# Kernel tuning notes

Measured on AMD Instinct MI355X. Metric: run time of the kernel, lower is better.

Reference implementation:

```python
import jax, jax.numpy as jnp
import numpy as np

B, L, D_MODEL, N_HEADS = 4, 2048, 1024, 16
HEAD_DIM = D_MODEL // N_HEADS


def setup_inputs() -> dict:
    key = jax.random.key(0)
    ks = jax.random.split(key, 11)
    s = 1.0 / np.sqrt(D_MODEL)
    return {
        "queries": jax.random.normal(ks[0], (B, L, D_MODEL), jnp.float32),
        "keys": jax.random.normal(ks[1], (B, L, D_MODEL), jnp.float32),
        "values": jax.random.normal(ks[2], (B, L, D_MODEL), jnp.float32),
        "Wq": jax.random.normal(ks[3], (D_MODEL, D_MODEL), jnp.float32) * s,
        "bq": jnp.zeros((D_MODEL,), jnp.float32),
        "Wk": jax.random.normal(ks[4], (D_MODEL, D_MODEL), jnp.float32) * s,
        "bk": jnp.zeros((D_MODEL,), jnp.float32),
        "Wv": jax.random.normal(ks[5], (D_MODEL, D_MODEL), jnp.float32) * s,
        "bv": jnp.zeros((D_MODEL,), jnp.float32),
        "Wo": jax.random.normal(ks[6], (D_MODEL, D_MODEL), jnp.float32) * s,
        "bo": jnp.zeros((D_MODEL,), jnp.float32),
    }


def reference(queries, keys, values, Wq, bq, Wk, bk, Wv, bv, Wo, bo):
    Bsz, Lq, _ = queries.shape
    S = keys.shape[1]
    H, E = N_HEADS, HEAD_DIM
    # QKV projections (weights stored [in, out])
    q = (queries @ Wq + bq).reshape(Bsz, Lq, H, E)
    k = (keys @ Wk + bk).reshape(Bsz, S, H, E)
    v = (values @ Wv + bv).reshape(Bsz, S, H, E)
    scale = 1.0 / np.sqrt(E)
    # scores: [B, H, L, S]
    scores = jnp.einsum("blhe,bshe->bhls", q, k)
    A = jax.nn.softmax(scale * scores, axis=-1)
    # context: [B, L, H, E] -> [B, L, D]
    ctx = jnp.einsum("bhls,bshd->blhd", A, v).reshape(Bsz, Lq, H * E)
    out = ctx @ Wo + bo
    return out
```

## Files before the change

### kernel.cpp

```cpp
#include <hip/hip_runtime.h>

#define BATCH 4
#define SEQ   2048
#define DMODEL 1024
#define NHEADS 16
#define HDIM  64
#define MROWS (BATCH * SEQ)

typedef float f32x4 __attribute__((ext_vector_type(4)));
typedef short s16x8 __attribute__((ext_vector_type(8)));
typedef short s16x4 __attribute__((ext_vector_type(4)));
typedef unsigned short u16;

#define MFMA32K(a, b, c) __builtin_amdgcn_mfma_f32_16x16x32_bf16((a), (b), (c), 0, 0, 0)
#define MFMA16K(a, b, c) __builtin_amdgcn_mfma_f32_16x16x16bf16_1k((a), (b), (c), 0, 0, 0)

__device__ __forceinline__ u16 f2bf(float x) {
    unsigned int u = __builtin_bit_cast(unsigned int, x);
    unsigned int r = u + 0x7fffu + ((u >> 16) & 1u);
    return (u16)(r >> 16);
}

#if __has_builtin(__builtin_amdgcn_cvt_pk_bf16_f32)
__device__ __forceinline__ unsigned int pack2bf(float a, float b) {
    auto r = __builtin_amdgcn_cvt_pk_bf16_f32(a, b);
    return __builtin_bit_cast(unsigned int, r);
}
#else
__device__ __forceinline__ unsigned int pack2bf(float a, float b) {
    return (unsigned int)f2bf(a) | ((unsigned int)f2bf(b) << 16);
}
#endif

__device__ __forceinline__ void dma16(const u16* g, const u16* l) {
    __builtin_amdgcn_global_load_lds(
        (const __attribute__((address_space(1))) unsigned int*)g,
        (__attribute__((address_space(3))) unsigned int*)l, 16, 0, 0);
}

__global__ __launch_bounds__(256) void convk3(
    const float* __restrict__ s0, const float* __restrict__ s1,
    const float* __restrict__ s2, u16* __restrict__ d0, u16* __restrict__ d1,
    u16* __restrict__ d2) {
    const int z = blockIdx.y;
    const float* src = (z == 0) ? s0 : (z == 1) ? s1 : s2;
    u16* dst = (z == 0) ? d0 : (z == 1) ? d1 : d2;
    const int i = blockIdx.x * 256 + threadIdx.x;
    float4 a = ((const float4*)src)[i * 2];
    float4 b = ((const float4*)src)[i * 2 + 1];
    uint4 o;
    o.x = pack2bf(a.x, a.y); o.y = pack2bf(a.z, a.w);
    o.z = pack2bf(b.x, b.y); o.w = pack2bf(b.z, b.w);
    *(uint4*)(dst + (size_t)i * 8) = o;
}

__global__ __launch_bounds__(256) void wconv(const float* __restrict__ W0,
                                             const float* __restrict__ W1,
                                             const float* __restrict__ W2,
                                             const float* __restrict__ W3,
                                             u16* __restrict__ Wt) {
    __shared__ u16 tile[64][80];
    const int t = threadIdx.x;
    const int mtx = blockIdx.z;
    const float* W = (mtx == 0) ? W0 : (mtx == 1) ? W1 : (mtx == 2) ? W2 : W3;
    u16* out = Wt + (size_t)mtx * DMODEL * DMODEL;
    const int n0 = blockIdx.x * 64, k0 = blockIdx.y * 64;
#pragma unroll
    for (int j = 0; j < 4; ++j) {
        int k = j * 16 + (t >> 4);
        int c = (t & 15) * 4;
        float4 v = *(const float4*)(W + (size_t)(k0 + k) * DMODEL + n0 + c);
        tile[c + 0][k] = f2bf(v.x);
        tile[c + 1][k] = f2bf(v.y);
        tile[c + 2][k] = f2bf(v.z);
        tile[c + 3][k] = f2bf(v.w);
    }
    __syncthreads();
#pragma unroll
    for (int i2 = 0; i2 < 2; ++i2) {
        int n = i2 * 32 + (t >> 3), ck = (t & 7) * 8;
        uint4 v = *(const uint4*)(&tile[n][ck]);
        *(uint4*)(out + (size_t)(n0 + n) * DMODEL + k0 + ck) = v;
    }
}

__global__ __launch_bounds__(256) void vtrans(const u16* __restrict__ vbuf,
                                              u16* __restrict__ vtg) {
    __shared__ u16 tile[64][72];
    const int t = threadIdx.x;
    const int s0 = blockIdx.x * 64, h = blockIdx.y, b = blockIdx.z;
#pragma unroll
    for (int i = 0; i < 2; ++i) {
        int idx = i * 256 + t;
        int srow = idx >> 3, un = idx & 7;
        union { uint4 v; u16 s[8]; } u;
        u.v = *(const uint4*)(vbuf + (size_t)(b * SEQ + s0 + srow) * DMODEL + h * HDIM + un * 8);
#pragma unroll
        for (int ii = 0; ii < 8; ++ii)
            tile[un * 8 + ii][srow] = u.s[ii];
    }
    __syncthreads();
#pragma unroll
    for (int i = 0; i < 2; ++i) {
        int idx = i * 256 + t;
        int e = idx >> 3, un = idx & 7;
        uint4 v = *(const uint4*)(&tile[e][un * 8]);
        *(uint4*)(vtg + ((size_t)((b * NHEADS + h) * HDIM + e)) * SEQ + s0 + un * 8) = v;
    }
}

__global__ __launch_bounds__(256) void gemm_qkv(
    const u16* __restrict__ Aq, const u16* __restrict__ Ak,
    const u16* __restrict__ Av, const u16* __restrict__ Wt,
    const float* __restrict__ biq, const float* __restrict__ bik,
    const float* __restrict__ biv, u16* __restrict__ oq, u16* __restrict__ ok,
    u16* __restrict__ ov, float sq) {
    __shared__ u16 As[128 * 32];
    __shared__ u16 Bs[128 * 32];
    const int t = threadIdx.x;
    const int w = t >> 6, lane = t & 63, quad = lane >> 4, l16 = lane & 15;
    const int z = blockIdx.z;
    const u16* A = (z == 0) ? Aq : (z == 1) ? Ak : Av;
    const u16* B = Wt + (size_t)z * DMODEL * DMODEL;
    const float* bias = (z == 0) ? biq : (z == 1) ? bik : biv;
    u16* C = (z == 0) ? oq : (z == 1) ? ok : ov;
    const float scale = (z == 0) ? sq : 1.0f;
    const int m0 = blockIdx.x * 128, n0 = blockIdx.y * 128;
    const int wm = (w >> 1) * 64, wn = (w & 1) * 64;
    const int lr = lane >> 2, lc = (lane & 3) * 8;

    f32x4 acc[4][4] = {};

    for (int k0 = 0; k0 < DMODEL; k0 += 32) {
#pragma unroll
        for (int j = 0; j < 2; ++j) {
            int row = w * 32 + j * 16;
            dma16(A + (size_t)(m0 + row + lr) * DMODEL + k0 + lc, &As[row * 32]);
            dma16(B + (size_t)(n0 + row + lr) * DMODEL + k0 + lc, &Bs[row * 32]);
        }
        __syncthreads();
        s16x8 af[4], bf[4];
#pragma unroll
        for (int mt = 0; mt < 4; ++mt)
            af[mt] = *(const s16x8*)(&As[(wm + mt * 16 + l16) * 32 + quad * 8]);
#pragma unroll
        for (int nt = 0; nt < 4; ++nt)
            bf[nt] = *(const s16x8*)(&Bs[(wn + nt * 16 + l16) * 32 + quad * 8]);
#pragma unroll
        for (int mt = 0; mt < 4; ++mt)
#pragma unroll
            for (int nt = 0; nt < 4; ++nt)
                acc[mt][nt] = MFMA32K(af[mt], bf[nt], acc[mt][nt]);
        __syncthreads();
    }

#pragma unroll
    for (int mt = 0; mt < 4; ++mt)
#pragma unroll
        for (int nt = 0; nt < 4; ++nt) {
            int col = n0 + wn + nt * 16 + l16;
            float bv_ = bias[col];
#pragma unroll
            for (int r = 0; r < 4; ++r) {
                int row = m0 + wm + mt * 16 + quad * 4 + r;
                C[(size_t)row * DMODEL + col] = f2bf((acc[mt][nt][r] + bv_) * scale);
            }
        }
}

__global__ __launch_bounds__(256) void gemm_o(const u16* __restrict__ A,
                                              const u16* __restrict__ Bt,
                                              const float* __restrict__ bias,
                                              float* __restrict__ Cp) {
    __shared__ u16 As[128 * 32];
    __shared__ u16 Bs[128 * 32];
    const int t = threadIdx.x;
    const int w = t >> 6, lane = t & 63, quad = lane >> 4, l16 = lane & 15;
    const int m0 = blockIdx.x * 128, n0 = blockIdx.y * 128;
    const int wm = (w >> 1) * 64, wn = (w & 1) * 64;
    const int lr = lane >> 2, lc = (lane & 3) * 8;

    f32x4 acc[4][4] = {};

    for (int k0 = 0; k0 < DMODEL; k0 += 32) {
#pragma unroll
        for (int j = 0; j < 2; ++j) {
            int row = w * 32 + j * 16;
            dma16(A + (size_t)(m0 + row + lr) * DMODEL + k0 + lc, &As[row * 32]);
            dma16(Bt + (size_t)(n0 + row + lr) * DMODEL + k0 + lc, &Bs[row * 32]);
        }
        __syncthreads();
        s16x8 af[4], bf[4];
#pragma unroll
        for (int mt = 0; mt < 4; ++mt)
            af[mt] = *(const s16x8*)(&As[(wm + mt * 16 + l16) * 32 + quad * 8]);
#pragma unroll
        for (int nt = 0; nt < 4; ++nt)
            bf[nt] = *(const s16x8*)(&Bs[(wn + nt * 16 + l16) * 32 + quad * 8]);
#pragma unroll
        for (int mt = 0; mt < 4; ++mt)
#pragma unroll
            for (int nt = 0; nt < 4; ++nt)
                acc[mt][nt] = MFMA32K(af[mt], bf[nt], acc[mt][nt]);
        __syncthreads();
    }

#pragma unroll
    for (int mt = 0; mt < 4; ++mt)
#pragma unroll
        for (int nt = 0; nt < 4; ++nt) {
            int col = n0 + wn + nt * 16 + l16;
            float bv_ = bias[col];
#pragma unroll
            for (int r = 0; r < 4; ++r) {
                int row = m0 + wm + mt * 16 + quad * 4 + r;
                Cp[(size_t)row * DMODEL + col] = acc[mt][nt][r] + bv_;
            }
        }
}

__global__ __launch_bounds__(256, 4) void attn3(const u16* __restrict__ qb,
                                                const u16* __restrict__ kb,
                                                const u16* __restrict__ vtg,
                                                u16* __restrict__ ctxb) {
    __shared__ u16 Ks[2][64 * 64];
    __shared__ u16 Vt[2][64 * 64];
    const int t = threadIdx.x;
    const int w = t >> 6, lane = t & 63, quad = lane >> 4, l16 = lane & 15;
    const int h = blockIdx.x, b = blockIdx.z, q0 = blockIdx.y * 128;

    s16x8 bq[2][2];
#pragma unroll
    for (int qs = 0; qs < 2; ++qs) {
        size_t base = (size_t)(b * SEQ + q0 + w * 32 + qs * 16 + l16) * DMODEL + h * HDIM + quad * 8;
        bq[qs][0] = *(const s16x8*)(qb + base);
        bq[qs][1] = *(const s16x8*)(qb + base + 32);
    }

    const int krow = lane >> 3;
    const int kunit = (lane & 7) ^ krow;
    const u16* vbase = vtg + (size_t)((b * NHEADS + h) * HDIM) * SEQ;

    float lsum[2] = {0.0f, 0.0f};
    f32x4 o[2][4] = {};

#define STAGE_KV(bf_, ss_)                                                              \
    do {                                                                                \
        _Pragma("unroll")                                                               \
        for (int j = 0; j < 2; ++j) {                                                   \
            int row = w * 16 + j * 8 + krow;                                            \
            dma16(kb + (size_t)(b * SEQ + (ss_) + row) * DMODEL + h * HDIM + kunit * 8, \
                  &Ks[bf_][(w * 16 + j * 8) * 64]);                                     \
            dma16(vbase + (size_t)row * SEQ + (ss_) + kunit * 8,                        \
                  &Vt[bf_][(w * 16 + j * 8) * 64]);                                     \
        }                                                                               \
    } while (0)

    STAGE_KV(0, 0);
    __syncthreads();

    const int NT = SEQ / 64;
    for (int tt = 0; tt < NT; ++tt) {
        const int buf = tt & 1;
        if (tt + 1 < NT) STAGE_KV(buf ^ 1, (tt + 1) * 64);

        s16x8 ak[4][2];
#pragma unroll
        for (int kt = 0; kt < 4; ++kt) {
            int row = kt * 16 + l16;
#pragma unroll
            for (int hf = 0; hf < 2; ++hf) {
                int un = (hf * 4 + quad) ^ (l16 & 7);
                ak[kt][hf] = *(const s16x8*)(&Ks[buf][row * 64 + un * 8]);
            }
        }

        s16x4 pf[2][4];
#pragma unroll
        for (int qs = 0; qs < 2; ++qs) {
            f32x4 sc[4];
            __builtin_amdgcn_s_setprio(1);
#pragma unroll
            for (int kt = 0; kt < 4; ++kt) {
                f32x4 zz = {0.0f, 0.0f, 0.0f, 0.0f};
                zz = MFMA32K(ak[kt][0], bq[qs][0], zz);
                sc[kt] = MFMA32K(ak[kt][1], bq[qs][1], zz);
            }
            __builtin_amdgcn_s_setprio(0);
            float rs = 0.0f;
            float p[4][4];
#pragma unroll
            for (int kt = 0; kt < 4; ++kt)
#pragma unroll
                for (int r = 0; r < 4; ++r) {
                    p[kt][r] = __builtin_amdgcn_exp2f(sc[kt][r]);
                    rs += p[kt][r];
                }
            rs += __shfl_xor(rs, 16);
            rs += __shfl_xor(rs, 32);
            lsum[qs] += rs;
#pragma unroll
            for (int kt = 0; kt < 4; ++kt) {
                union { unsigned int u[2]; s16x4 v; } pb;
                pb.u[0] = pack2bf(p[kt][0], p[kt][1]);
                pb.u[1] = pack2bf(p[kt][2], p[kt][3]);
                pf[qs][kt] = pb.v;
            }
        }

#pragma unroll
        for (int mt = 0; mt < 4; ++mt) {
            const int dim = mt * 16 + l16;
            const u16* vrow = &Vt[buf][dim * 64 + ((quad & 1) << 2)];
            const int sw = l16 & 7;
#pragma unroll
            for (int kt = 0; kt < 4; ++kt) {
                int un = (kt * 2 + (quad >> 1)) ^ sw;
                s16x4 av = *(const s16x4*)(vrow + un * 8);
                __builtin_amdgcn_s_setprio(1);
#pragma unroll
                for (int qs = 0; qs < 2; ++qs)
                    o[qs][mt] = MFMA16K(av, pf[qs][kt], o[qs][mt]);
                __builtin_amdgcn_s_setprio(0);
            }
        }
        __syncthreads();
    }
#undef STAGE_KV

#pragma unroll
    for (int qs = 0; qs < 2; ++qs) {
        float rl = 1.0f / lsum[qs];
        size_t rowbase = (size_t)(b * SEQ + q0 + w * 32 + qs * 16 + l16) * DMODEL + h * HDIM;
#pragma unroll
        for (int mt = 0; mt < 4; ++mt)
#pragma unroll
            for (int rr = 0; rr < 2; ++rr) {
                unsigned int v = pack2bf(o[qs][mt][rr * 2] * rl, o[qs][mt][rr * 2 + 1] * rl);
                *(unsigned int*)(&ctxb[rowbase + mt * 16 + quad * 4 + rr * 2]) = v;
            }
    }
}

extern "C" void kernel_launch(void* const* d_in, const int* in_sizes, int n_in,
                              void* d_out, int out_size, void* d_ws, size_t ws_size,
                              hipStream_t stream) {
    const float* queries = (const float*)d_in[0];
    const float* keys    = (const float*)d_in[1];
    const float* values  = (const float*)d_in[2];
    const float* Wq = (const float*)d_in[3];
    const float* bq = (const float*)d_in[4];
    const float* Wk = (const float*)d_in[5];
    const float* bk = (const float*)d_in[6];
    const float* Wv = (const float*)d_in[7];
    const float* bv = (const float*)d_in[8];
    const float* Wo = (const float*)d_in[9];
    const float* bo = (const float*)d_in[10];
    float* out = (float*)d_out;

    char* ws = (char*)d_ws;
    u16* Wt   = (u16*)ws;
    u16* aq   = (u16*)(ws + ((size_t)8 << 20));
    u16* ak   = (u16*)(ws + ((size_t)24 << 20));
    u16* av   = (u16*)(ws + ((size_t)40 << 20));
    u16* qbuf = (u16*)(ws + ((size_t)56 << 20));
    u16* kbuf = (u16*)(ws + ((size_t)72 << 20));
    u16* vbuf = (u16*)(ws + ((size_t)88 << 20));
    u16* ctxb = qbuf;
    u16* vtg  = av;

    const size_t WSZ = (size_t)DMODEL * DMODEL;
    const float S2 = 0.125f * 1.44269504088896340736f;

    dim3 blk(256);

    wconv<<<dim3(16, 16, 4), blk, 0, stream>>>(Wq, Wk, Wv, Wo, Wt);
    convk3<<<dim3(4096, 3), blk, 0, stream>>>(queries, keys, values, aq, ak, av);

    gemm_qkv<<<dim3(64, 8, 3), blk, 0, stream>>>(aq, ak, av, Wt,
                                                 bq, bk, bv, qbuf, kbuf, vbuf, S2);

    vtrans<<<dim3(SEQ / 64, NHEADS, BATCH), blk, 0, stream>>>(vbuf, vtg);

    attn3<<<dim3(NHEADS, SEQ / 128, BATCH), blk, 0, stream>>>(qbuf, kbuf, vtg, ctxb);

    gemm_o<<<dim3(64, 8), blk, 0, stream>>>(ctxb, Wt + 3 * WSZ, bo, out);
}
```

Before: 425.5 us.

## Fuse V transpose into attention kernel via register-staged LDS transpose

Removes the standalone vtrans kernel. The attention kernel now loads V rows directly from the projection output into registers, prefetching the next tile during compute, and scatters them transposed into a padded, swizzled LDS buffer after the PV MFMAs. This drops one launch and a global round trip of V, but adds per-element 16-bit LDS stores, a padded shared buffer, and register pressure in the hot loop in place of the async DMA of pre-transposed V.

```diff
diff --git a/kernel.cpp b/kernel.cpp
--- a/kernel.cpp
+++ b/kernel.cpp
@@ -81,31 +81,6 @@
         int n = i2 * 32 + (t >> 3), ck = (t & 7) * 8;
         uint4 v = *(const uint4*)(&tile[n][ck]);
         *(uint4*)(out + (size_t)(n0 + n) * DMODEL + k0 + ck) = v;
-    }
-}
-
-__global__ __launch_bounds__(256) void vtrans(const u16* __restrict__ vbuf,
-                                              u16* __restrict__ vtg) {
-    __shared__ u16 tile[64][72];
-    const int t = threadIdx.x;
-    const int s0 = blockIdx.x * 64, h = blockIdx.y, b = blockIdx.z;
-#pragma unroll
-    for (int i = 0; i < 2; ++i) {
-        int idx = i * 256 + t;
-        int srow = idx >> 3, un = idx & 7;
-        union { uint4 v; u16 s[8]; } u;
-        u.v = *(const uint4*)(vbuf + (size_t)(b * SEQ + s0 + srow) * DMODEL + h * HDIM + un * 8);
-#pragma unroll
-        for (int ii = 0; ii < 8; ++ii)
-            tile[un * 8 + ii][srow] = u.s[ii];
-    }
-    __syncthreads();
-#pragma unroll
-    for (int i = 0; i < 2; ++i) {
-        int idx = i * 256 + t;
-        int e = idx >> 3, un = idx & 7;
-        uint4 v = *(const uint4*)(&tile[e][un * 8]);
-        *(uint4*)(vtg + ((size_t)((b * NHEADS + h) * HDIM + e)) * SEQ + s0 + un * 8) = v;
     }
 }
 
@@ -221,10 +196,10 @@
 
 __global__ __launch_bounds__(256, 4) void attn3(const u16* __restrict__ qb,
                                                 const u16* __restrict__ kb,
-                                                const u16* __restrict__ vtg,
+                                                const u16* __restrict__ vb,
                                                 u16* __restrict__ ctxb) {
     __shared__ u16 Ks[2][64 * 64];
-    __shared__ u16 Vt[2][64 * 64];
+    __shared__ u16 Vt[2][64 * 72];
     const int t = threadIdx.x;
     const int w = t >> 6, lane = t & 63, quad = lane >> 4, l16 = lane & 15;
     const int h = blockIdx.x, b = blockIdx.z, q0 = blockIdx.y * 128;
@@ -238,31 +213,63 @@
     }
 
     const int krow = lane >> 3;
-    const int kunit = (lane & 7) ^ krow;
-    const u16* vbase = vtg + (size_t)((b * NHEADS + h) * HDIM) * SEQ;
+    const int kunit = (lane & 7) ^ (krow & 7);
+
+    int vkey[2], vseg[2], vcol[2];
+    const u16* vsrc[2];
+#pragma unroll
+    for (int i = 0; i < 2; ++i) {
+        int idx = i * 256 + t;
+        vkey[i] = idx >> 3;
+        vseg[i] = idx & 7;
+        vcol[i] = (((vkey[i] >> 3) ^ vseg[i]) << 3) + (vkey[i] & 7);
+        vsrc[i] = vb + (size_t)(b * SEQ + vkey[i]) * DMODEL + h * HDIM + vseg[i] * 8;
+    }
 
     float lsum[2] = {0.0f, 0.0f};
     f32x4 o[2][4] = {};
-
-#define STAGE_KV(bf_, ss_)                                                              \
+    uint4 vld[2];
+
+#define STAGE_K(bf_, ss_)                                                               \
     do {                                                                                \
         _Pragma("unroll")                                                               \
         for (int j = 0; j < 2; ++j) {                                                   \
             int row = w * 16 + j * 8 + krow;                                            \
             dma16(kb + (size_t)(b * SEQ + (ss_) + row) * DMODEL + h * HDIM + kunit * 8, \
                   &Ks[bf_][(w * 16 + j * 8) * 64]);                                     \
-            dma16(vbase + (size_t)row * SEQ + (ss_) + kunit * 8,                        \
-                  &Vt[bf_][(w * 16 + j * 8) * 64]);                                     \
         }                                                                               \
     } while (0)
 
-    STAGE_KV(0, 0);
+#define VLOAD(ss_)                                                                      \
+    do {                                                                                \
+        vld[0] = *(const uint4*)(vsrc[0] + (size_t)(ss_)*DMODEL);                       \
+        vld[1] = *(const uint4*)(vsrc[1] + (size_t)(ss_)*DMODEL);                       \
+    } while (0)
+
+#define VSTORE(bf_)                                                                     \
+    do {                                                                                \
+        _Pragma("unroll")                                                               \
+        for (int i = 0; i < 2; ++i) {                                                   \
+            union { uint4 v; u16 s[8]; } u_;                                            \
+            u_.v = vld[i];                                                              \
+            _Pragma("unroll")                                                           \
+            for (int ii = 0; ii < 8; ++ii)                                              \
+                Vt[bf_][(vseg[i] * 8 + ii) * 72 + vcol[i]] = u_.s[ii];                  \
+        }                                                                               \
+    } while (0)
+
+    STAGE_K(0, 0);
+    VLOAD(0);
+    VSTORE(0);
     __syncthreads();
 
     const int NT = SEQ / 64;
     for (int tt = 0; tt < NT; ++tt) {
         const int buf = tt & 1;
-        if (tt + 1 < NT) STAGE_KV(buf ^ 1, (tt + 1) * 64);
+        if (tt + 1 < NT) {
+            STAGE_K(buf ^ 1, (tt + 1) * 64);
+            VLOAD((tt + 1) * 64);
+        }
 
         s16x8 ak[4][2];
 #pragma unroll
@@ -311,12 +318,12 @@
 #pragma unroll
         for (int mt = 0; mt < 4; ++mt) {
             const int dim = mt * 16 + l16;
-            const u16* vrow = &Vt[buf][dim * 64 + ((quad & 1) << 2)];
-            const int sw = l16 & 7;
+            const int swz = (dim >> 3) & 7;
+            const int rowoff = dim * 72;
 #pragma unroll
             for (int kt = 0; kt < 4; ++kt) {
-                int un = (kt * 2 + (quad >> 1)) ^ sw;
-                s16x4 av = *(const s16x4*)(vrow + un * 8);
+                int col = ((((kt * 2) + (quad >> 1)) ^ swz) << 3) + ((quad & 1) << 2);
+                s16x4 av = *(const s16x4*)(&Vt[buf][rowoff + col]);
                 __builtin_amdgcn_s_setprio(1);
 #pragma unroll
                 for (int qs = 0; qs < 2; ++qs)
@@ -324,9 +331,13 @@
                 __builtin_amdgcn_s_setprio(0);
             }
         }
-        __syncthreads();
-    }
-#undef STAGE_KV
+
+        if (tt + 1 < NT) VSTORE(buf ^ 1);
+        __syncthreads();
+    }
+#undef STAGE_K
+#undef VLOAD
+#undef VSTORE
 
 #pragma unroll
     for (int qs = 0; qs < 2; ++qs) {
@@ -367,7 +378,6 @@
     u16* kbuf = (u16*)(ws + ((size_t)72 << 20));
     u16* vbuf = (u16*)(ws + ((size_t)88 << 20));
     u16* ctxb = qbuf;
-    u16* vtg  = av;
 
     const size_t WSZ = (size_t)DMODEL * DMODEL;
     const float S2 = 0.125f * 1.44269504088896340736f;
@@ -380,9 +390,7 @@
     gemm_qkv<<<dim3(64, 8, 3), blk, 0, stream>>>(aq, ak, av, Wt,
                                                  bq, bk, bv, qbuf, kbuf, vbuf, S2);
 
-    vtrans<<<dim3(SEQ / 64, NHEADS, BATCH), blk, 0, stream>>>(vbuf, vtg);
-
-    attn3<<<dim3(NHEADS, SEQ / 128, BATCH), blk, 0, stream>>>(qbuf, kbuf, vtg, ctxb);
+    attn3<<<dim3(NHEADS, SEQ / 128, BATCH), blk, 0, stream>>>(qbuf, kbuf, vbuf, ctxb);
 
     gemm_o<<<dim3(64, 8), blk, 0, stream>>>(ctxb, Wt + 3 * WSZ, bo, out);
 }
```

Result: slower. 636.8 us (+49.7%).
